# Kernel tuning notes

Measured on AMD Instinct MI355X. Metric: run time of the kernel, lower is better.

Reference implementation:

```python
import jax, jax.numpy as jnp
import numpy as np
from jax import lax

B, N, D = 4, 4096, 1024
H, DH, K = 8, 128, 256  # heads, dim_head, linformer k
KERNEL = 32
PAD = (15, 16)  # torch padding='same' for even kernel: left=(k-1)//2, right=rest


def setup_inputs() -> dict:
    key = jax.random.key(0)
    ks = jax.random.split(key, 7)
    s = 0.02
    return {
        "x": jax.random.normal(ks[0], (B, N, D), dtype=jnp.float32),
        "Wq": jax.random.normal(ks[1], (D, D), dtype=jnp.float32) * s,
        "Wk": jax.random.normal(ks[2], (D, D), dtype=jnp.float32) * s,
        "Wpk": jax.random.normal(ks[3], (K, N, KERNEL), dtype=jnp.float32) * s,
        "bpk": jax.random.normal(ks[4], (K,), dtype=jnp.float32) * s,
        "Wo": jax.random.normal(ks[5], (D, D), dtype=jnp.float32) * s,
        "bo": jax.random.normal(ks[6], (D,), dtype=jnp.float32) * s,
    }


def reference(x, Wq, Wk, Wpk, bpk, Wo, bo):
    b, n, d = x.shape
    # linear projections (torch Linear: y = x @ W.T)
    q = x @ Wq.T                       # (b, n, h*dh)
    keys = x @ Wk.T                    # (b, n, h*dh)
    # Conv1d over feature length with seq positions as channels: (b, n, d) -> (b, k, d)
    keys = lax.conv_general_dilated(
        keys, Wpk, window_strides=(1,), padding=[PAD],
        dimension_numbers=("NCH", "OIH", "NCH"),
    ) + bpk[None, :, None]             # (b, K, h*dh)
    values = keys                      # share_kv=True
    # split heads
    q = q.reshape(b, n, H, DH).transpose(0, 2, 1, 3)        # (b, h, n, dh)
    kk = keys.reshape(b, K, H, DH).transpose(0, 2, 1, 3)    # (b, h, K, dh)
    vv = values.reshape(b, K, H, DH).transpose(0, 2, 1, 3)  # (b, h, K, dh)
    dots = jnp.einsum("bhnd,bhkd->bhnk", q, kk) * (DH ** -0.5)
    attn = jax.nn.softmax(dots, axis=-1)                    # dropout p=0.0 (eval)
    out = jnp.einsum("bhnk,bhkd->bhnd", attn, vv)
    out = out.transpose(0, 2, 1, 3).reshape(b, n, H * DH)
    return out @ Wo.T + bo
```

## Files before the change

kernel.cpp:

```cpp
#include <hip/hip_runtime.h>


typedef short v8s __attribute__((ext_vector_type(8)));
typedef float v4f __attribute__((ext_vector_type(4)));

#define MFMA16(a, b, c) __builtin_amdgcn_mfma_f32_16x16x32_bf16((a), (b), (c), 0, 0, 0)
#define WAITV(N) asm volatile("s_waitcnt vmcnt(" #N ")" ::: "memory")
#define SBAR() __builtin_amdgcn_s_barrier()

__device__ __forceinline__ unsigned short f2bf(float f) {
  unsigned int u = __float_as_uint(f);
  u += 0x7fffu + ((u >> 16) & 1u);
  return (unsigned short)(u >> 16);
}

__device__ __forceinline__ v8s cvt8(float4 a, float4 b) {
  v8s v;
  v[0] = (short)f2bf(a.x); v[1] = (short)f2bf(a.y);
  v[2] = (short)f2bf(a.z); v[3] = (short)f2bf(a.w);
  v[4] = (short)f2bf(b.x); v[5] = (short)f2bf(b.y);
  v[6] = (short)f2bf(b.z); v[7] = (short)f2bf(b.w);
  return v;
}

__device__ __forceinline__ void gld16(void* lds, const void* g) {
  __builtin_amdgcn_global_load_lds(
      (const __attribute__((address_space(1))) void*)g,
      (__attribute__((address_space(3))) void*)lds, 16, 0, 0);
}

__device__ __forceinline__ const v8s* frag_ptr(const short* base, int row, int g) {
  return (const v8s*)(base + row * 32 + (((g ^ (row >> 1)) & 3) << 3));
}

__global__ __launch_bounds__(256) void k_cvt(const float* __restrict__ src,
                                             short* __restrict__ dst, int n8) {
  const int i = blockIdx.x * 256 + threadIdx.x;
  if (i >= n8) return;
  const float4* s = (const float4*)src;
  ((v8s*)dst)[i] = cvt8(s[2 * i], s[2 * i + 1]);
}

__global__ __launch_bounds__(256) void k_reorder_wpk(const float* __restrict__ Wpk,
                                                     short* __restrict__ Wr) {
  __shared__ short T[64][40];
  const int k  = blockIdx.x >> 6;
  const int n0 = (blockIdx.x & 63) << 6;
  const int tid = threadIdx.x;
  {
    const int i = tid >> 2, t0 = (tid & 3) << 3;
    const float* p = Wpk + ((size_t)k * 4096 + n0 + i) * 32 + t0;
    float4 a = *(const float4*)p, b = *(const float4*)(p + 4);
    *(v8s*)&T[i][t0] = cvt8(a, b);
  }
  __syncthreads();
  {
    const int t = tid >> 3, j0 = (tid & 7) << 3;
    v8s o;
#pragma unroll
    for (int q = 0; q < 8; ++q) o[q] = T[j0 + q][t];
    *(v8s*)(Wr + ((size_t)t * 256 + k) * 4096 + n0 + j0) = o;
  }
}

__global__ __launch_bounds__(256) void k_zero_pad(short* __restrict__ KpTp) {
  const int idx = blockIdx.x * 256 + threadIdx.x;
  const int ridx = idx >> 9, col8 = idx & 511;
  const int b = ridx >> 5, rr = ridx & 31;
  const int row = (rr < 15) ? rr : 1039 + (rr - 15);
  v8s z = {0, 0, 0, 0, 0, 0, 0, 0};
  *(v8s*)(KpTp + ((size_t)b * 1056 + row) * 4096 + col8 * 8) = z;
}

__global__ __launch_bounds__(256, 2) void k_gemm_qk_v4(const short* __restrict__ xbf,
                                                       const short* __restrict__ Wqk,
                                                       short* __restrict__ Qbf,
                                                       short* __restrict__ Kp) {
  __shared__ short As[2][256][32];
  __shared__ short Bs[2][128][32];
  const int tid = threadIdx.x, lane = tid & 63, w = tid >> 6;
  const int m0 = blockIdx.x * 256, j0 = blockIdx.y * 128;
  const int wm = w * 64;
  const int l15 = lane & 15, g = lane >> 4;
  const int lr = lane >> 2, lseg = lane & 3;

  v4f acc[4][8];
#pragma unroll
  for (int i = 0; i < 4; ++i)
#pragma unroll
    for (int j = 0; j < 8; ++j) acc[i][j] = (v4f)0.0f;

  auto stage = [&](int buf, int k0) {
#pragma unroll
    for (int q = 0; q < 4; ++q) {
      const int rblk = q * 64 + w * 16, r = rblk + lr;
      const int co = ((lseg ^ (r >> 1)) & 3) << 3;
      gld16(&As[buf][rblk][0], xbf + (size_t)(m0 + r) * 1024 + k0 + co);
    }
#pragma unroll
    for (int q = 0; q < 2; ++q) {
      const int rblk = q * 64 + w * 16, r = rblk + lr;
      const int co = ((lseg ^ (r >> 1)) & 3) << 3;
      gld16(&Bs[buf][rblk][0], Wqk + (size_t)(j0 + r) * 1024 + k0 + co);
    }
  };

  stage(0, 0);
#pragma unroll 1
  for (int p = 0, buf = 0; p < 32; ++p, buf ^= 1) {
    if (p + 1 < 32) stage(buf ^ 1, (p + 1) * 32);
    if (p < 31) { WAITV(6); } else { WAITV(0); }
    SBAR();
    v8s af[4];
#pragma unroll
    for (int mi = 0; mi < 4; ++mi)
      af[mi] = *frag_ptr(&As[buf][0][0], wm + mi * 16 + l15, g);
    __builtin_amdgcn_s_setprio(1);
#pragma unroll
    for (int nh = 0; nh < 2; ++nh) {
      v8s bq[4];
#pragma unroll
      for (int nj = 0; nj < 4; ++nj)
        bq[nj] = *frag_ptr(&Bs[buf][0][0], nh * 64 + nj * 16 + l15, g);
#pragma unroll
      for (int nj = 0; nj < 4; ++nj)
#pragma unroll
        for (int mi = 0; mi < 4; ++mi)
          acc[mi][nh * 4 + nj] = MFMA16(af[mi], bq[nj], acc[mi][nh * 4 + nj]);
    }
    __builtin_amdgcn_s_setprio(0);
    SBAR();
  }
  const int rbase = g * 4;
#pragma unroll
  for (int mi = 0; mi < 4; ++mi)
#pragma unroll
    for (int nf = 0; nf < 8; ++nf) {
      const int col = j0 + nf * 16 + l15;
      short* dst = (col < 1024) ? Qbf : Kp;
      const int cj = (col < 1024) ? col : col - 1024;
#pragma unroll
      for (int r = 0; r < 4; ++r) {
        const int row = m0 + wm + mi * 16 + rbase + r;
        dst[(size_t)row * 1024 + cj] = (short)f2bf(acc[mi][nf][r]);
      }
    }
}

__global__ __launch_bounds__(256) void k_transpose_pad(const short* __restrict__ src,
                                                       short* __restrict__ dst) {
  __shared__ short T[64][72];
  const int r0 = blockIdx.x * 64, c0 = blockIdx.y * 64, b = blockIdx.z;
  const int tid = threadIdx.x;
  {
    const int i = tid >> 2, q = (tid & 3) << 4;
    const short* ps = src + ((size_t)b * 4096 + r0 + i) * 1024 + c0 + q;
    *(v8s*)&T[i][q]     = *(const v8s*)ps;
    *(v8s*)&T[i][q + 8] = *(const v8s*)(ps + 8);
  }
  __syncthreads();
  {
    const int j = tid >> 2, p = (tid & 3) << 4;
    v8s o0, o1;
#pragma unroll
    for (int t = 0; t < 8; ++t) o0[t] = T[p + t][j];
#pragma unroll
    for (int t = 0; t < 8; ++t) o1[t] = T[p + 8 + t][j];
    short* pd = dst + ((size_t)b * 1056 + 15 + c0 + j) * 4096 + r0 + p;
    *(v8s*)pd = o0;
    *(v8s*)(pd + 8) = o1;
  }
}

__global__ __launch_bounds__(256, 2) void k_conv_v6(const short* __restrict__ Wr,
                                                    const short* __restrict__ KpTp,
                                                    float* __restrict__ Pq) {
  __shared__ short A[3][256][32];
  __shared__ short Kt[2][160][32];
  const int bid = blockIdx.x;
  const int ns = (bid & 7) | (((bid >> 8) & 1) << 3);
  const int j  = (bid >> 3) & 31;
  const int b = j >> 3, nt = j & 7;
  const int D0 = nt * 128;
  const int nbase = ns * 256;
  const int tid = threadIdx.x, lane = tid & 63, w = tid >> 6;
  const int wm = w * 64;
  const int l15 = lane & 15, g = lane >> 4;
  const int lr = lane >> 2, lseg = lane & 3;
  const short* KpTb = KpTp + (size_t)b * 1056 * 4096;

  v4f acc[4][8];
#pragma unroll
  for (int mi = 0; mi < 4; ++mi)
#pragma unroll
    for (int ni = 0; ni < 8; ++ni) acc[mi][ni] = (v4f)0.0f;

  auto stageA = [&](int buf, int s2) {
    const int t2 = s2 & 31, c2 = s2 >> 5;
#pragma unroll
    for (int q = 0; q < 4; ++q) {
      const int rblk = q * 64 + w * 16, row = rblk + lr;
      const int sg = ((lseg ^ (row >> 1)) & 3) << 3;
      gld16(&A[buf][rblk][0],
            Wr + ((size_t)t2 * 256 + row) * 4096 + nbase + c2 * 32 + sg);
    }
  };
  auto stageKt = [&](int buf, int c1) {
#pragma unroll
    for (int q = 0; q < 2; ++q) {
      const int rblk = q * 64 + w * 16, row = rblk + lr;
      const int sg = ((lseg ^ (row >> 1)) & 3) << 3;
      gld16(&Kt[buf][rblk][0],
            KpTb + (size_t)(D0 + row) * 4096 + nbase + c1 * 32 + sg);
    }
    {
      const int rblk = 128 + (w & 1) * 16, row = rblk + lr;
      const int srow = row < 159 ? row : 158;
      const int sg = ((lseg ^ (row >> 1)) & 3) << 3;
      gld16(&Kt[buf][rblk][0],
            KpTb + (size_t)(D0 + srow) * 4096 + nbase + c1 * 32 + sg);
    }
  };

  stageA(0, 0);
  stageKt(0, 0);
  stageA(1, 1);
  WAITV(4);
  SBAR();

#pragma unroll 1
  for (int s = 0; s < 256; ++s) {
    const int t = s & 31, c = s >> 5;
    const int ab = s % 3;
    const short* Abp = &A[ab][0][0];
    const short* Ktp = &Kt[c & 1][0][0];
    const bool doKt = (t == 26) && (c < 7);
    if (s + 2 < 256) stageA((s + 2) % 3, s + 2);
    if (doKt) stageKt((c + 1) & 1, c + 1);
    v8s af[4];
#pragma unroll
    for (int mi = 0; mi < 4; ++mi)
      af[mi] = *frag_ptr(Abp, wm + mi * 16 + l15, g);
    __builtin_amdgcn_s_setprio(1);
#pragma unroll
    for (int nh = 0; nh < 2; ++nh) {
      v8s bq[4];
#pragma unroll
      for (int nj = 0; nj < 4; ++nj)
        bq[nj] = *frag_ptr(Ktp, nh * 64 + nj * 16 + l15 + t, g);
#pragma unroll
      for (int nj = 0; nj < 4; ++nj)
#pragma unroll
        for (int mi = 0; mi < 4; ++mi)
          acc[mi][nh * 4 + nj] = MFMA16(af[mi], bq[nj], acc[mi][nh * 4 + nj]);
    }
    __builtin_amdgcn_s_setprio(0);
    if (s < 254) {
      if (doKt) { WAITV(7); } else { WAITV(4); }
    } else if (s == 254) {
      WAITV(0);
    }
    SBAR();
  }

  float* Pp = Pq + (size_t)(ns * 4 + b) * 262144;
#pragma unroll
  for (int mi = 0; mi < 4; ++mi)
#pragma unroll
    for (int nf = 0; nf < 8; ++nf) {
      const int col = D0 + nf * 16 + l15;
#pragma unroll
      for (int r = 0; r < 4; ++r)
        Pp[(size_t)(wm + mi * 16 + g * 4 + r) * 1024 + col] = acc[mi][nf][r];
    }
}

__global__ __launch_bounds__(256) void k_reduce_kc(const float* __restrict__ P,
                                                   const float* __restrict__ bpk,
                                                   float* __restrict__ Kc) {
  const int i = (blockIdx.x * 256 + threadIdx.x) * 4;
  const float bias = bpk[(i >> 10) & 255];
  float4 s; s.x = bias; s.y = bias; s.z = bias; s.w = bias;
#pragma unroll
  for (int ns = 0; ns < 16; ++ns) {
    float4 v = *(const float4*)(P + (size_t)ns * 1048576 + i);
    s.x += v.x; s.y += v.y; s.z += v.z; s.w += v.w;
  }
  *(float4*)(Kc + i) = s;
}

__global__ __launch_bounds__(256) void k_kc_post(const float* __restrict__ Kc,
                                                 short* __restrict__ Kcbf,
                                                 short* __restrict__ KcT) {
  __shared__ short T[64][72];
  const int k0 = blockIdx.x * 64, d0 = blockIdx.y * 64, b = blockIdx.z;
  const int tid = threadIdx.x;
  {
    const int i = tid >> 2, q = (tid & 3) << 4;
    const float* ps = Kc + (size_t)(b * 256 + k0 + i) * 1024 + d0 + q;
    float4 f0 = *(const float4*)ps,       f1 = *(const float4*)(ps + 4);
    float4 f2 = *(const float4*)(ps + 8), f3 = *(const float4*)(ps + 12);
    v8s v0 = cvt8(f0, f1), v1 = cvt8(f2, f3);
    *(v8s*)&T[i][q] = v0;
    *(v8s*)&T[i][q + 8] = v1;
    short* pc = Kcbf + (size_t)(b * 256 + k0 + i) * 1024 + d0 + q;
    *(v8s*)pc = v0;
    *(v8s*)(pc + 8) = v1;
  }
  __syncthreads();
  {
    const int j = tid >> 2, p = (tid & 3) << 4;
    v8s o0, o1;
#pragma unroll
    for (int t = 0; t < 8; ++t) o0[t] = T[p + t][j];
#pragma unroll
    for (int t = 0; t < 8; ++t) o1[t] = T[p + 8 + t][j];
    short* pd = KcT + (size_t)(b * 1024 + d0 + j) * 256 + k0 + p;
    *(v8s*)pd = o0;
    *(v8s*)(pd + 8) = o1;
  }
}

__global__ __launch_bounds__(256) void k_attn(const short* __restrict__ Qbf,
                                              const short* __restrict__ Kcbf,
                                              const short* __restrict__ KcT,
                                              short* __restrict__ AO) {
  __shared__ short P[4][16][264];
  const int nt = blockIdx.x, h = blockIdx.y, b = blockIdx.z;
  const int tid = threadIdx.x, lane = tid & 63, w = tid >> 6;
  const int l15 = lane & 15, lg4 = (lane >> 4) * 4, lg8 = (lane >> 4) * 8;
  const float scale = 0.08838834764831845f;
  const size_t qb  = (size_t)b * 4096 * 1024 + (size_t)h * 128;
  const size_t kb  = (size_t)b * 256 * 1024 + (size_t)h * 128;
  const size_t vtb = ((size_t)b * 1024 + (size_t)h * 128) * 256;
  short (*Pw)[264] = P[w];
  const int n_wave = nt * 128 + w * 32;

#pragma unroll 1
  for (int half = 0; half < 2; ++half) {
    const int nbase = n_wave + half * 16;
    v8s aq[4];
#pragma unroll
    for (int kt = 0; kt < 4; ++kt)
      aq[kt] = *(const v8s*)(Qbf + qb + (size_t)(nbase + l15) * 1024 + kt * 32 + lg8);

    v4f dacc[16];
#pragma unroll
    for (int ct = 0; ct < 16; ++ct) dacc[ct] = (v4f)0.0f;
#pragma unroll 1
    for (int kt = 0; kt < 4; ++kt) {
#pragma unroll
      for (int ct = 0; ct < 16; ++ct) {
        v8s bk = *(const v8s*)(Kcbf + kb + (size_t)(ct * 16 + l15) * 1024 + kt * 32 + lg8);
        dacc[ct] = MFMA16(aq[kt], bk, dacc[ct]);
      }
    }
#pragma unroll
    for (int ct = 0; ct < 16; ++ct) dacc[ct] = dacc[ct] * scale;
    v4f m4 = dacc[0];
#pragma unroll
    for (int ct = 1; ct < 16; ++ct)
#pragma unroll
      for (int r = 0; r < 4; ++r) m4[r] = fmaxf(m4[r], dacc[ct][r]);
#pragma unroll
    for (int off = 1; off < 16; off <<= 1)
#pragma unroll
      for (int r = 0; r < 4; ++r) m4[r] = fmaxf(m4[r], __shfl_xor(m4[r], off, 64));
    v4f ssum = (v4f)0.0f;
#pragma unroll
    for (int ct = 0; ct < 16; ++ct)
#pragma unroll
      for (int r = 0; r < 4; ++r) {
        const float e = __expf(dacc[ct][r] - m4[r]);
        ssum[r] += e;
        Pw[lg4 + r][ct * 16 + l15] = (short)f2bf(e);
      }
#pragma unroll
    for (int off = 1; off < 16; off <<= 1)
#pragma unroll
      for (int r = 0; r < 4; ++r) ssum[r] += __shfl_xor(ssum[r], off, 64);
    __syncthreads();

    v4f oacc[8];
#pragma unroll
    for (int ct = 0; ct < 8; ++ct) oacc[ct] = (v4f)0.0f;
#pragma unroll 1
    for (int kt2 = 0; kt2 < 8; ++kt2) {
      v8s pa = *(const v8s*)&Pw[l15][kt2 * 32 + lg8];
#pragma unroll
      for (int ct = 0; ct < 8; ++ct) {
        v8s bv = *(const v8s*)(KcT + vtb + (size_t)(ct * 16 + l15) * 256 + kt2 * 32 + lg8);
        oacc[ct] = MFMA16(pa, bv, oacc[ct]);
      }
    }
    v4f inv;
#pragma unroll
    for (int r = 0; r < 4; ++r) inv[r] = 1.0f / ssum[r];
#pragma unroll
    for (int ct = 0; ct < 8; ++ct)
#pragma unroll
      for (int r = 0; r < 4; ++r)
        AO[qb + (size_t)(nbase + lg4 + r) * 1024 + ct * 16 + l15] =
            (short)f2bf(oacc[ct][r] * inv[r]);
    __syncthreads();
  }
}

__global__ __launch_bounds__(256) void k_gemm_out_v3(const short* __restrict__ AO,
                                                     const short* __restrict__ Wobf,
                                                     const float* __restrict__ bo,
                                                     float* __restrict__ out) {
  __shared__ short As[2][128][32];
  __shared__ short Bs[2][128][32];
  const int tid = threadIdx.x, lane = tid & 63, w = tid >> 6;
  const int m0 = blockIdx.x * 128, j0 = blockIdx.y * 128;
  const int wr = (w >> 1) * 64, wc = (w & 1) * 64;
  const int l15 = lane & 15, g = lane >> 4;
  const int sr = lane >> 2, sseg = lane & 3;

  v4f acc[4][4];
#pragma unroll
  for (int i = 0; i < 4; ++i)
#pragma unroll
    for (int j = 0; j < 4; ++j) acc[i][j] = (v4f)0.0f;

  auto stage = [&](int buf, int k0) {
#pragma unroll
    for (int q0 = 0; q0 < 2; ++q0) {
      const int rblk = (w * 2 + q0) << 4, r = rblk + sr;
      const int co = ((sseg ^ (r >> 1)) & 3) << 3;
      gld16(&As[buf][rblk][0], AO + (size_t)(m0 + r) * 1024 + k0 + co);
      gld16(&Bs[buf][rblk][0], Wobf + (size_t)(j0 + r) * 1024 + k0 + co);
    }
  };

  stage(0, 0);
#pragma unroll 1
  for (int p = 0, buf = 0; p < 32; ++p, buf ^= 1) {
    if (p + 1 < 32) stage(buf ^ 1, (p + 1) * 32);
    if (p < 31) { WAITV(4); } else { WAITV(0); }
    SBAR();
    v8s af[4], bf4[4];
#pragma unroll
    for (int mi = 0; mi < 4; ++mi)
      af[mi] = *frag_ptr(&As[buf][0][0], wr + mi * 16 + l15, g);
#pragma unroll
    for (int ni = 0; ni < 4; ++ni)
      bf4[ni] = *frag_ptr(&Bs[buf][0][0], wc + ni * 16 + l15, g);
#pragma unroll
    for (int ni = 0; ni < 4; ++ni)
#pragma unroll
      for (int mi = 0; mi < 4; ++mi)
        acc[mi][ni] = MFMA16(af[mi], bf4[ni], acc[mi][ni]);
    SBAR();
  }
  const int rbase = (lane >> 4) * 4;
#pragma unroll
  for (int mi = 0; mi < 4; ++mi)
#pragma unroll
    for (int ni = 0; ni < 4; ++ni) {
      const int col = j0 + wc + ni * 16 + l15;
      const float bias = bo[col];
#pragma unroll
      for (int r = 0; r < 4; ++r) {
        const int row = m0 + wr + mi * 16 + rbase + r;
        out[(size_t)row * 1024 + col] = acc[mi][ni][r] + bias;
      }
    }
}

extern "C" void kernel_launch(void* const* d_in, const int* in_sizes, int n_in,
                              void* d_out, int out_size, void* d_ws, size_t ws_size,
                              hipStream_t stream) {
  const float* x   = (const float*)d_in[0];
  const float* Wq  = (const float*)d_in[1];
  const float* Wk  = (const float*)d_in[2];
  const float* Wpk = (const float*)d_in[3];
  const float* bpk = (const float*)d_in[4];
  const float* Wo  = (const float*)d_in[5];
  const float* bo  = (const float*)d_in[6];

  const size_t OFF_WR   = 0;
  const size_t OFF_XBF  = 67108864;
  const size_t OFF_WQK  = 100663296;
  const size_t OFF_KPTP = 67108864;
  const size_t OFF_KCBF = 67108864;
  const size_t OFF_KCT  = 69206016;
  const size_t OFF_WOBF = 101711872;
  const size_t OFF_QBF  = 104857600;
  const size_t OFF_KP   = 138412032;
  const size_t OFF_KC   = 171966464;
  const size_t NEED     = 176160768;
  if (ws_size < NEED) return;

  char* ws = (char*)d_ws;
  short* Wr   = (short*)(ws + OFF_WR);
  short* xbf  = (short*)(ws + OFF_XBF);
  short* Wqk  = (short*)(ws + OFF_WQK);
  short* KpTp = (short*)(ws + OFF_KPTP);
  short* Kcbf = (short*)(ws + OFF_KCBF);
  short* KcT  = (short*)(ws + OFF_KCT);
  short* Wobf = (short*)(ws + OFF_WOBF);
  short* Qbf  = (short*)(ws + OFF_QBF);
  short* Kp   = (short*)(ws + OFF_KP);
  float* Kc   = (float*)(ws + OFF_KC);
  short* AO   = Kp;
  float* Ppart = (float*)d_out;
  float* outp = (float*)d_out;

  k_cvt<<<dim3(8192), dim3(256), 0, stream>>>(x, xbf, 16777216 / 8);
  k_cvt<<<dim3(512),  dim3(256), 0, stream>>>(Wq, Wqk, 1048576 / 8);
  k_cvt<<<dim3(512),  dim3(256), 0, stream>>>(Wk, Wqk + 1048576, 1048576 / 8);
  k_reorder_wpk<<<dim3(16384), dim3(256), 0, stream>>>(Wpk, Wr);
  k_gemm_qk_v4<<<dim3(64, 16), dim3(256), 0, stream>>>(xbf, Wqk, Qbf, Kp);
  k_transpose_pad<<<dim3(64, 16, 4), dim3(256), 0, stream>>>(Kp, KpTp);
  k_cvt<<<dim3(512), dim3(256), 0, stream>>>(Wo, Wobf, 1048576 / 8);
  k_zero_pad<<<dim3(256), dim3(256), 0, stream>>>(KpTp);
  k_conv_v6<<<dim3(512), dim3(256), 0, stream>>>(Wr, KpTp, Ppart);
  k_reduce_kc<<<dim3(1024), dim3(256), 0, stream>>>(Ppart, bpk, Kc);
  k_kc_post<<<dim3(4, 16, 4), dim3(256), 0, stream>>>(Kc, Kcbf, KcT);
  k_attn<<<dim3(32, 8, 4), dim3(256), 0, stream>>>(Qbf, Kcbf, KcT, AO);
  k_gemm_out_v3<<<dim3(128, 8), dim3(256), 0, stream>>>(AO, Wobf, bo, outp);
}
```

Measured before the change: 664.5 us.

## Load conv A fragments directly from global into registers, use 8 waves

```diff
diff --git a/kernel.cpp b/kernel.cpp
--- a/kernel.cpp
+++ b/kernel.cpp
@@ -172,10 +172,9 @@
   }
 }
 
-__global__ __launch_bounds__(256, 2) void k_conv_v6(const short* __restrict__ Wr,
+__global__ __launch_bounds__(512, 4) void k_conv_v7(const short* __restrict__ Wr,
                                                     const short* __restrict__ KpTp,
                                                     float* __restrict__ Pq) {
-  __shared__ short A[3][256][32];
   __shared__ short Kt[2][160][32];
   const int bid = blockIdx.x;
   const int ns = (bid & 7) | (((bid >> 8) & 1) << 3);
@@ -184,37 +183,28 @@
   const int D0 = nt * 128;
   const int nbase = ns * 256;
   const int tid = threadIdx.x, lane = tid & 63, w = tid >> 6;
-  const int wm = w * 64;
+  const int wm = (w >> 1) * 64, wn = (w & 1) * 64;
   const int l15 = lane & 15, g = lane >> 4;
   const int lr = lane >> 2, lseg = lane & 3;
   const short* KpTb = KpTp + (size_t)b * 1056 * 4096;
 
-  v4f acc[4][8];
+  v4f acc[4][4];
 #pragma unroll
   for (int mi = 0; mi < 4; ++mi)
 #pragma unroll
-    for (int ni = 0; ni < 8; ++ni) acc[mi][ni] = (v4f)0.0f;
-
-  auto stageA = [&](int buf, int s2) {
-    const int t2 = s2 & 31, c2 = s2 >> 5;
-#pragma unroll
-    for (int q = 0; q < 4; ++q) {
-      const int rblk = q * 64 + w * 16, row = rblk + lr;
-      const int sg = ((lseg ^ (row >> 1)) & 3) << 3;
-      gld16(&A[buf][rblk][0],
-            Wr + ((size_t)t2 * 256 + row) * 4096 + nbase + c2 * 32 + sg);
-    }
+    for (int ni = 0; ni < 4; ++ni) acc[mi][ni] = (v4f)0.0f;
+
+  const short* Abase = Wr + (size_t)(wm + l15) * 4096 + nbase + g * 8;
+  auto ldA = [&](int s, int mi) -> v8s {
+    const int t = s & 31, c = s >> 5;
+    return *(const v8s*)(Abase + ((size_t)t * 256 + mi * 16) * 4096 + c * 32);
   };
   auto stageKt = [&](int buf, int c1) {
-#pragma unroll
-    for (int q = 0; q < 2; ++q) {
-      const int rblk = q * 64 + w * 16, row = rblk + lr;
-      const int sg = ((lseg ^ (row >> 1)) & 3) << 3;
-      gld16(&Kt[buf][rblk][0],
-            KpTb + (size_t)(D0 + row) * 4096 + nbase + c1 * 32 + sg);
-    }
-    {
-      const int rblk = 128 + (w & 1) * 16, row = rblk + lr;
+    const int q1 = w, q2 = (w < 2) ? 8 + w : w;
+#pragma unroll
+    for (int pass = 0; pass < 2; ++pass) {
+      const int q = pass ? q2 : q1;
+      const int rblk = q * 16, row = rblk + lr;
       const int srow = row < 159 ? row : 158;
       const int sg = ((lseg ^ (row >> 1)) & 3) << 3;
       gld16(&Kt[buf][rblk][0],
@@ -222,56 +212,48 @@
     }
   };
 
-  stageA(0, 0);
   stageKt(0, 0);
-  stageA(1, 1);
-  WAITV(4);
+  v8s afc[4], afn[4];
+#pragma unroll
+  for (int mi = 0; mi < 4; ++mi) afc[mi] = ldA(0, mi);
+  WAITV(0);
   SBAR();
 
 #pragma unroll 1
   for (int s = 0; s < 256; ++s) {
     const int t = s & 31, c = s >> 5;
-    const int ab = s % 3;
-    const short* Abp = &A[ab][0][0];
+    if (s + 1 < 256) {
+#pragma unroll
+      for (int mi = 0; mi < 4; ++mi) afn[mi] = ldA(s + 1, mi);
+    }
+    if (t == 26 && c < 7) stageKt((c + 1) & 1, c + 1);
     const short* Ktp = &Kt[c & 1][0][0];
-    const bool doKt = (t == 26) && (c < 7);
-    if (s + 2 < 256) stageA((s + 2) % 3, s + 2);
-    if (doKt) stageKt((c + 1) & 1, c + 1);
-    v8s af[4];
-#pragma unroll
-    for (int mi = 0; mi < 4; ++mi)
-      af[mi] = *frag_ptr(Abp, wm + mi * 16 + l15, g);
+    v8s bq[4];
+#pragma unroll
+    for (int nj = 0; nj < 4; ++nj)
+      bq[nj] = *frag_ptr(Ktp, wn + nj * 16 + l15 + t, g);
     __builtin_amdgcn_s_setprio(1);
 #pragma unroll
-    for (int nh = 0; nh < 2; ++nh) {
-      v8s bq[4];
-#pragma unroll
-      for (int nj = 0; nj < 4; ++nj)
-        bq[nj] = *frag_ptr(Ktp, nh * 64 + nj * 16 + l15 + t, g);
-#pragma unroll
-      for (int nj = 0; nj < 4; ++nj)
-#pragma unroll
-        for (int mi = 0; mi < 4; ++mi)
-          acc[mi][nh * 4 + nj] = MFMA16(af[mi], bq[nj], acc[mi][nh * 4 + nj]);
-    }
+    for (int ni = 0; ni < 4; ++ni)
+#pragma unroll
+      for (int mi = 0; mi < 4; ++mi)
+        acc[mi][ni] = MFMA16(afc[mi], bq[ni], acc[mi][ni]);
     __builtin_amdgcn_s_setprio(0);
-    if (s < 254) {
-      if (doKt) { WAITV(7); } else { WAITV(4); }
-    } else if (s == 254) {
-      WAITV(0);
-    }
+    if (t == 31) { WAITV(4); }
     SBAR();
+#pragma unroll
+    for (int mi = 0; mi < 4; ++mi) afc[mi] = afn[mi];
   }
 
   float* Pp = Pq + (size_t)(ns * 4 + b) * 262144;
 #pragma unroll
   for (int mi = 0; mi < 4; ++mi)
 #pragma unroll
-    for (int nf = 0; nf < 8; ++nf) {
-      const int col = D0 + nf * 16 + l15;
+    for (int ni = 0; ni < 4; ++ni) {
+      const int col = D0 + wn + ni * 16 + l15;
 #pragma unroll
       for (int r = 0; r < 4; ++r)
-        Pp[(size_t)(wm + mi * 16 + g * 4 + r) * 1024 + col] = acc[mi][nf][r];
+        Pp[(size_t)(wm + mi * 16 + g * 4 + r) * 1024 + col] = acc[mi][ni][r];
     }
 }
 
@@ -516,7 +498,7 @@
   k_transpose_pad<<<dim3(64, 16, 4), dim3(256), 0, stream>>>(Kp, KpTp);
   k_cvt<<<dim3(512), dim3(256), 0, stream>>>(Wo, Wobf, 1048576 / 8);
   k_zero_pad<<<dim3(256), dim3(256), 0, stream>>>(KpTp);
-  k_conv_v6<<<dim3(512), dim3(256), 0, stream>>>(Wr, KpTp, Ppart);
+  k_conv_v7<<<dim3(512), dim3(512), 0, stream>>>(Wr, KpTp, Ppart);
   k_reduce_kc<<<dim3(1024), dim3(256), 0, stream>>>(Ppart, bpk, Kc);
   k_kc_post<<<dim3(4, 16, 4), dim3(256), 0, stream>>>(Kc, Kcbf, KcT);
   k_attn<<<dim3(32, 8, 4), dim3(256), 0, stream>>>(Qbf, Kcbf, KcT, AO);
```

After: 838.4 us. 1.26x slower.

## Split conv tile across 8 waves and enlarge output GEMM tile to 256x128

Applied to the files above, without the earlier changes.

```diff
diff --git a/kernel.cpp b/kernel.cpp
--- a/kernel.cpp
+++ b/kernel.cpp
@@ -172,7 +172,7 @@
   }
 }
 
-__global__ __launch_bounds__(256, 2) void k_conv_v6(const short* __restrict__ Wr,
+__global__ __launch_bounds__(512, 4) void k_conv_v5(const short* __restrict__ Wr,
                                                     const short* __restrict__ KpTp,
                                                     float* __restrict__ Pq) {
   __shared__ short A[3][256][32];
@@ -184,94 +184,84 @@
   const int D0 = nt * 128;
   const int nbase = ns * 256;
   const int tid = threadIdx.x, lane = tid & 63, w = tid >> 6;
-  const int wm = w * 64;
+  const int wm = (w >> 1) * 64, wn = (w & 1) * 64;
   const int l15 = lane & 15, g = lane >> 4;
   const int lr = lane >> 2, lseg = lane & 3;
   const short* KpTb = KpTp + (size_t)b * 1056 * 4096;
 
-  v4f acc[4][8];
+  v4f acc[4][4];
 #pragma unroll
   for (int mi = 0; mi < 4; ++mi)
 #pragma unroll
-    for (int ni = 0; ni < 8; ++ni) acc[mi][ni] = (v4f)0.0f;
-
-  auto stageA = [&](int buf, int s2) {
+    for (int ni = 0; ni < 4; ++ni) acc[mi][ni] = (v4f)0.0f;
+
+  auto stageA = [&](int buf, int s2, int q) {
     const int t2 = s2 & 31, c2 = s2 >> 5;
-#pragma unroll
-    for (int q = 0; q < 4; ++q) {
-      const int rblk = q * 64 + w * 16, row = rblk + lr;
-      const int sg = ((lseg ^ (row >> 1)) & 3) << 3;
-      gld16(&A[buf][rblk][0],
-            Wr + ((size_t)t2 * 256 + row) * 4096 + nbase + c2 * 32 + sg);
-    }
+    const int rblk = q * 128 + w * 16;
+    const int row = rblk + lr;
+    const int sg = ((lseg ^ (row >> 1)) & 3) << 3;
+    gld16(&A[buf][rblk][0],
+          Wr + ((size_t)t2 * 256 + row) * 4096 + nbase + c2 * 32 + sg);
   };
-  auto stageKt = [&](int buf, int c1) {
-#pragma unroll
-    for (int q = 0; q < 2; ++q) {
-      const int rblk = q * 64 + w * 16, row = rblk + lr;
-      const int sg = ((lseg ^ (row >> 1)) & 3) << 3;
-      gld16(&Kt[buf][rblk][0],
-            KpTb + (size_t)(D0 + row) * 4096 + nbase + c1 * 32 + sg);
-    }
-    {
-      const int rblk = 128 + (w & 1) * 16, row = rblk + lr;
-      const int srow = row < 159 ? row : 158;
-      const int sg = ((lseg ^ (row >> 1)) & 3) << 3;
-      gld16(&Kt[buf][rblk][0],
-            KpTb + (size_t)(D0 + srow) * 4096 + nbase + c1 * 32 + sg);
-    }
+  auto stageKt = [&](int buf, int c1, int q) {
+    const int rblk = q * 128 + w * 16;
+    const int row = rblk + lr;
+    const int srow = row < 159 ? row : 158;
+    const int sg = ((lseg ^ (row >> 1)) & 3) << 3;
+    gld16(&Kt[buf][rblk][0],
+          KpTb + (size_t)(D0 + srow) * 4096 + nbase + c1 * 32 + sg);
   };
 
-  stageA(0, 0);
-  stageKt(0, 0);
-  stageA(1, 1);
-  WAITV(4);
+  stageA(0, 0, 0); stageA(0, 0, 1);
+  stageKt(0, 0, 0);
+  if (w < 2) stageKt(0, 0, 1);
+  stageA(1, 1, 0); stageA(1, 1, 1);
+  WAITV(2);
   SBAR();
 
+  int ab = 0, pab = 2;
 #pragma unroll 1
   for (int s = 0; s < 256; ++s) {
     const int t = s & 31, c = s >> 5;
-    const int ab = s % 3;
     const short* Abp = &A[ab][0][0];
     const short* Ktp = &Kt[c & 1][0][0];
-    const bool doKt = (t == 26) && (c < 7);
-    if (s + 2 < 256) stageA((s + 2) % 3, s + 2);
-    if (doKt) stageKt((c + 1) & 1, c + 1);
-    v8s af[4];
+    v8s aq[4], bq[4];
 #pragma unroll
     for (int mi = 0; mi < 4; ++mi)
-      af[mi] = *frag_ptr(Abp, wm + mi * 16 + l15, g);
+      aq[mi] = *frag_ptr(Abp, wm + mi * 16 + l15, g);
+#pragma unroll
+    for (int ni = 0; ni < 4; ++ni)
+      bq[ni] = *frag_ptr(Ktp, wn + ni * 16 + l15 + t, g);
+    if (s + 2 < 256) { stageA(pab, s + 2, 0); stageA(pab, s + 2, 1); }
+    const bool kt0 = (t == 26) && (c < 7);
+    const bool kt1 = (t == 27) && (c < 7);
+    if (kt0) stageKt((c + 1) & 1, c + 1, 0);
+    if (kt1 && w < 2) stageKt((c + 1) & 1, c + 1, 1);
     __builtin_amdgcn_s_setprio(1);
 #pragma unroll
-    for (int nh = 0; nh < 2; ++nh) {
-      v8s bq[4];
-#pragma unroll
-      for (int nj = 0; nj < 4; ++nj)
-        bq[nj] = *frag_ptr(Ktp, nh * 64 + nj * 16 + l15 + t, g);
-#pragma unroll
-      for (int nj = 0; nj < 4; ++nj)
-#pragma unroll
-        for (int mi = 0; mi < 4; ++mi)
-          acc[mi][nh * 4 + nj] = MFMA16(af[mi], bq[nj], acc[mi][nh * 4 + nj]);
-    }
+    for (int ni = 0; ni < 4; ++ni)
+#pragma unroll
+      for (int mi = 0; mi < 4; ++mi)
+        acc[mi][ni] = MFMA16(aq[mi], bq[ni], acc[mi][ni]);
     __builtin_amdgcn_s_setprio(0);
     if (s < 254) {
-      if (doKt) { WAITV(7); } else { WAITV(4); }
+      if (kt0 || kt1) { WAITV(3); } else { WAITV(2); }
     } else if (s == 254) {
       WAITV(0);
     }
     SBAR();
+    pab = ab; ab = (ab == 2) ? 0 : ab + 1;
   }
 
   float* Pp = Pq + (size_t)(ns * 4 + b) * 262144;
 #pragma unroll
   for (int mi = 0; mi < 4; ++mi)
 #pragma unroll
-    for (int nf = 0; nf < 8; ++nf) {
-      const int col = D0 + nf * 16 + l15;
+    for (int ni = 0; ni < 4; ++ni) {
+      const int col = D0 + wn + ni * 16 + l15;
 #pragma unroll
       for (int r = 0; r < 4; ++r)
-        Pp[(size_t)(wm + mi * 16 + g * 4 + r) * 1024 + col] = acc[mi][nf][r];
+        Pp[(size_t)(wm + mi * 16 + g * 4 + r) * 1024 + col] = acc[mi][ni][r];
     }
 }
 
@@ -406,30 +396,35 @@
   }
 }
 
-__global__ __launch_bounds__(256) void k_gemm_out_v3(const short* __restrict__ AO,
-                                                     const short* __restrict__ Wobf,
-                                                     const float* __restrict__ bo,
-                                                     float* __restrict__ out) {
-  __shared__ short As[2][128][32];
+__global__ __launch_bounds__(256, 2) void k_gemm_out_v4(const short* __restrict__ AO,
+                                                        const short* __restrict__ Wobf,
+                                                        const float* __restrict__ bo,
+                                                        float* __restrict__ out) {
+  __shared__ short As[2][256][32];
   __shared__ short Bs[2][128][32];
   const int tid = threadIdx.x, lane = tid & 63, w = tid >> 6;
-  const int m0 = blockIdx.x * 128, j0 = blockIdx.y * 128;
-  const int wr = (w >> 1) * 64, wc = (w & 1) * 64;
+  const int m0 = blockIdx.x * 256, j0 = blockIdx.y * 128;
+  const int wm = w * 64;
   const int l15 = lane & 15, g = lane >> 4;
-  const int sr = lane >> 2, sseg = lane & 3;
-
-  v4f acc[4][4];
+  const int lr = lane >> 2, lseg = lane & 3;
+
+  v4f acc[4][8];
 #pragma unroll
   for (int i = 0; i < 4; ++i)
 #pragma unroll
-    for (int j = 0; j < 4; ++j) acc[i][j] = (v4f)0.0f;
+    for (int j = 0; j < 8; ++j) acc[i][j] = (v4f)0.0f;
 
   auto stage = [&](int buf, int k0) {
 #pragma unroll
-    for (int q0 = 0; q0 < 2; ++q0) {
-      const int rblk = (w * 2 + q0) << 4, r = rblk + sr;
-      const int co = ((sseg ^ (r >> 1)) & 3) << 3;
+    for (int q = 0; q < 4; ++q) {
+      const int rblk = q * 64 + w * 16, r = rblk + lr;
+      const int co = ((lseg ^ (r >> 1)) & 3) << 3;
       gld16(&As[buf][rblk][0], AO + (size_t)(m0 + r) * 1024 + k0 + co);
+    }
+#pragma unroll
+    for (int q = 0; q < 2; ++q) {
+      const int rblk = q * 64 + w * 16, r = rblk + lr;
+      const int co = ((lseg ^ (r >> 1)) & 3) << 3;
       gld16(&Bs[buf][rblk][0], Wobf + (size_t)(j0 + r) * 1024 + k0 + co);
     }
   };
@@ -438,33 +433,39 @@
 #pragma unroll 1
   for (int p = 0, buf = 0; p < 32; ++p, buf ^= 1) {
     if (p + 1 < 32) stage(buf ^ 1, (p + 1) * 32);
-    if (p < 31) { WAITV(4); } else { WAITV(0); }
+    if (p < 31) { WAITV(6); } else { WAITV(0); }
     SBAR();
-    v8s af[4], bf4[4];
+    v8s af[4];
 #pragma unroll
     for (int mi = 0; mi < 4; ++mi)
-      af[mi] = *frag_ptr(&As[buf][0][0], wr + mi * 16 + l15, g);
-#pragma unroll
-    for (int ni = 0; ni < 4; ++ni)
-      bf4[ni] = *frag_ptr(&Bs[buf][0][0], wc + ni * 16 + l15, g);
-#pragma unroll
-    for (int ni = 0; ni < 4; ++ni)
-#pragma unroll
-      for (int mi = 0; mi < 4; ++mi)
-        acc[mi][ni] = MFMA16(af[mi], bf4[ni], acc[mi][ni]);
+      af[mi] = *frag_ptr(&As[buf][0][0], wm + mi * 16 + l15, g);
+    __builtin_amdgcn_s_setprio(1);
+#pragma unroll
+    for (int nh = 0; nh < 2; ++nh) {
+      v8s bq[4];
+#pragma unroll
+      for (int nj = 0; nj < 4; ++nj)
+        bq[nj] = *frag_ptr(&Bs[buf][0][0], nh * 64 + nj * 16 + l15, g);
+#pragma unroll
+      for (int nj = 0; nj < 4; ++nj)
+#pragma unroll
+        for (int mi = 0; mi < 4; ++mi)
+          acc[mi][nh * 4 + nj] = MFMA16(af[mi], bq[nj], acc[mi][nh * 4 + nj]);
+    }
+    __builtin_amdgcn_s_setprio(0);
     SBAR();
   }
-  const int rbase = (lane >> 4) * 4;
+  const int rbase = g * 4;
 #pragma unroll
   for (int mi = 0; mi < 4; ++mi)
 #pragma unroll
-    for (int ni = 0; ni < 4; ++ni) {
-      const int col = j0 + wc + ni * 16 + l15;
+    for (int nf = 0; nf < 8; ++nf) {
+      const int col = j0 + nf * 16 + l15;
       const float bias = bo[col];
 #pragma unroll
       for (int r = 0; r < 4; ++r) {
-        const int row = m0 + wr + mi * 16 + rbase + r;
-        out[(size_t)row * 1024 + col] = acc[mi][ni][r] + bias;
+        const int row = m0 + wm + mi * 16 + rbase + r;
+        out[(size_t)row * 1024 + col] = acc[mi][nf][r] + bias;
       }
     }
 }
@@ -516,9 +517,9 @@
   k_transpose_pad<<<dim3(64, 16, 4), dim3(256), 0, stream>>>(Kp, KpTp);
   k_cvt<<<dim3(512), dim3(256), 0, stream>>>(Wo, Wobf, 1048576 / 8);
   k_zero_pad<<<dim3(256), dim3(256), 0, stream>>>(KpTp);
-  k_conv_v6<<<dim3(512), dim3(256), 0, stream>>>(Wr, KpTp, Ppart);
+  k_conv_v5<<<dim3(512), dim3(512), 0, stream>>>(Wr, KpTp, Ppart);
   k_reduce_kc<<<dim3(1024), dim3(256), 0, stream>>>(Ppart, bpk, Kc);
   k_kc_post<<<dim3(4, 16, 4), dim3(256), 0, stream>>>(Kc, Kcbf, KcT);
   k_attn<<<dim3(32, 8, 4), dim3(256), 0, stream>>>(Qbf, Kcbf, KcT, AO);
-  k_gemm_out_v3<<<dim3(128, 8), dim3(256), 0, stream>>>(AO, Wobf, bo, outp);
-}
+  k_gemm_out_v4<<<dim3(64, 8), dim3(256), 0, stream>>>(AO, Wobf, bo, outp);
+}
```

Result: faster. 598.5 us (-9.9%).
